# Performance work log

Hardware: AMD Instinct MI355X
Metric: run time of the kernel (lower is better)

## Reference

```python
import jax, jax.numpy as jnp
import numpy as np

# --- constants matching init_kwargs / input_specs ---
B, T, N, C = 16, 60, 196, 512
SEGS, TOP_K, TOP_M = 10, 6, 12
HEADS = 4
HD = C // HEADS  # 128
CLIP = T // SEGS  # 6
FRAMES = CLIP * TOP_K  # 36
LN_EPS = 1e-5


def setup_inputs() -> dict:
    key = jax.random.key(0)
    ks = jax.random.split(key, 16)
    s = 0.02
    return {
        "audio_feat": jax.random.normal(ks[0], (B, T, C), jnp.float32),
        "patch_feat": jax.random.normal(ks[1], (B, T, N, C), jnp.float32),
        "qst_feat": jax.random.normal(ks[2], (B, C), jnp.float32),
        "top_k_index_sort": jnp.sort(jax.random.randint(ks[3], (B, 1, TOP_K), 0, SEGS), axis=-1),
        # MultiheadAttention params (torch layout: in_proj [3C, C])
        "in_proj_w": jax.random.normal(ks[4], (3 * C, C), jnp.float32) * s,
        "in_proj_b": jnp.zeros((3 * C,), jnp.float32),
        "out_w": jax.random.normal(ks[5], (C, C), jnp.float32) * s,
        "out_b": jnp.zeros((C,), jnp.float32),
        # FFN
        "lin1_w": jax.random.normal(ks[6], (C, C), jnp.float32) * s,
        "lin1_b": jnp.zeros((C,), jnp.float32),
        "lin2_w": jax.random.normal(ks[7], (C, C), jnp.float32) * s,
        "lin2_b": jnp.zeros((C,), jnp.float32),
        # LayerNorm
        "ln_g": jnp.ones((C,), jnp.float32),
        "ln_b": jnp.zeros((C,), jnp.float32),
    }


def _layernorm(x, g, b):
    mu = jnp.mean(x, axis=-1, keepdims=True)
    var = jnp.mean(jnp.square(x - mu), axis=-1, keepdims=True)
    return (x - mu) * jax.lax.rsqrt(var + LN_EPS) * g + b


def _forward(audio_feat, patch_feat, qst_feat, top_k_index_sort,
             in_proj_w, in_proj_b, out_w, out_b,
             lin1_w, lin1_b, lin2_w, lin2_b, ln_g, ln_b):
    # --- TopKSegs: gather top-k temporal segments (clip_len frames each) ---
    seg_idx = top_k_index_sort[:, 0, :]  # [B, K]
    frame_ids = (seg_idx[:, :, None] * CLIP + jnp.arange(CLIP)[None, None, :]).reshape(B, FRAMES)
    audio_top_k = jnp.take_along_axis(audio_feat, frame_ids[:, :, None], axis=1)            # [B, F, C]
    patch_top_k = jnp.take_along_axis(patch_feat, frame_ids[:, :, None, None], axis=1)      # [B, F, N, C]

    # --- QstQueryPatchAttn: batched cross-attention (q_len=1 per frame) ---
    Wq, Wk, Wv = in_proj_w[:C], in_proj_w[C:2 * C], in_proj_w[2 * C:]
    bq, bk, bv = in_proj_b[:C], in_proj_b[C:2 * C], in_proj_b[2 * C:]
    q = (qst_feat @ Wq.T + bq).reshape(B, HEADS, HD)                    # [B, h, d]
    k = (patch_top_k @ Wk.T + bk).reshape(B, FRAMES, N, HEADS, HD)      # [B, F, N, h, d]
    v = (patch_top_k @ Wv.T + bv).reshape(B, FRAMES, N, HEADS, HD)
    scale = 1.0 / jnp.sqrt(jnp.asarray(HD, jnp.float32))
    scores = jnp.einsum('bhd,bfnhd->bfhn', q, k) * scale                # [B, F, h, N]
    w = jax.nn.softmax(scores, axis=-1)
    ctx = jnp.einsum('bfhn,bfnhd->bfhd', w, v).reshape(B, FRAMES, C)
    attn_feat = ctx @ out_w.T + out_b                                   # [B, F, C]
    patch_weights = jnp.mean(w, axis=2)                                 # [B, F, N] (avg heads)

    src = jax.nn.relu(attn_feat @ lin1_w.T + lin1_b) @ lin2_w.T + lin2_b
    visual_spatial_feat = _layernorm(attn_feat + src, ln_g, ln_b)       # computed but unused downstream

    # --- SelectTopM (faithful to original loop semantics):
    # top-m indices are sorted ascending and iterated with full-slab overwrite,
    sort_index = jnp.argsort(patch_weights, axis=-1)
    top_m_index = sort_index[:, :, -TOP_M:]
    top_m_index_sort = jnp.sort(top_m_index, axis=-1)
    pid = top_m_index_sort[0, 0, -1]  # last iterated patch id
    sel = jnp.take(patch_top_k, pid, axis=2)                            # [B, F, C]
    visual_patch_top_m = jnp.broadcast_to(sel[:, :, None, :], (B, FRAMES, TOP_M, C))
    visual_patch_feat = visual_patch_top_m.reshape(B, FRAMES * TOP_M, C)
    return audio_top_k, visual_patch_top_m, visual_patch_feat


def reference(audio_feat, patch_feat, qst_feat, top_k_index_sort,
              in_proj_w, in_proj_b, out_w, out_b,
              lin1_w, lin1_b, lin2_w, lin2_b, ln_g, ln_b):
    return _forward(audio_feat, patch_feat, qst_feat, top_k_index_sort,
                    in_proj_w, in_proj_b, out_w, out_b,
                    lin1_w, lin1_b, lin2_w, lin2_b, ln_g, ln_b)
```

## Files before the change

kernel.cpp:

```cpp
#include <hip/hip_runtime.h>
#include <math.h>

#define B_     16
#define T_     60
#define N_     196
#define C_     512
#define SEGS_  10
#define TOPK_  6
#define TOPM_  12
#define HEADS_ 4
#define HD_    128
#define CLIP_  6
#define FRAMES_ 36

#define WS_Q    0
#define WS_SCP  512
#define WS_PID  2080

#define SCALE_ 0.08838834764831845f

__global__ void qproj_kernel(const float* __restrict__ qst,
                             const float* __restrict__ ipw,
                             const float* __restrict__ ipb,
                             float* __restrict__ ws) {
    __shared__ float x[C_];
    int tid = threadIdx.x;
    x[tid]       = qst[tid];
    x[tid + 256] = qst[tid + 256];
    __syncthreads();

    int wave = tid >> 6, lane = tid & 63;
    int half = lane >> 5, l = lane & 31;
    int row = blockIdx.x * 8 + wave * 2 + half;

    const float4* w4 = (const float4*)(ipw + (size_t)row * C_);
    const float4* x4 = (const float4*)x;
    float acc = 0.f;
    #pragma unroll
    for (int j = 0; j < 4; ++j) {
        float4 wv = w4[l + 32 * j];
        float4 xv = x4[l + 32 * j];
        acc += wv.x * xv.x + wv.y * xv.y + wv.z * xv.z + wv.w * xv.w;
    }
    for (int off = 16; off; off >>= 1) acc += __shfl_xor(acc, off);
    if (l == 0) ws[WS_Q + row] = acc + ipb[row];
}

__global__ void score_kernel(const float* __restrict__ patch,
                             const int* __restrict__ tk,
                             const float* __restrict__ ipw,
                             float* __restrict__ ws) {
    __shared__ float qh[HD_];
    __shared__ float us[256];
    int tid = threadIdx.x;
    int h = blockIdx.x >> 1, half = blockIdx.x & 1;
    int c = half * 256 + tid;

    if (tid < HD_) qh[tid] = ws[WS_Q + h * HD_ + tid];
    __syncthreads();

    const float* wk = ipw + (size_t)(C_ + h * HD_) * C_ + c;
    float u = 0.f;
    #pragma unroll 16
    for (int d = 0; d < HD_; ++d) u += qh[d] * wk[(size_t)d * C_];
    us[tid] = u;
    __syncthreads();

    int fid0 = tk[0] * CLIP_;
    const float* pb = patch + (size_t)fid0 * N_ * C_ + half * 256;
    int wave = tid >> 6, lane = tid & 63;
    const float4* u4 = (const float4*)us;
    float4 uv = u4[lane];
    for (int n = wave; n < N_; n += 4) {
        const float4* x4 = (const float4*)(pb + (size_t)n * C_);
        float4 xv = x4[lane];
        float p = uv.x * xv.x + uv.y * xv.y + uv.z * xv.z + uv.w * xv.w;
        for (int off = 32; off; off >>= 1) p += __shfl_down(p, off);
        if (lane == 0)
            ws[WS_SCP + (size_t)blockIdx.x * N_ + n] = p * SCALE_;
    }
}

__global__ void pid_kernel(float* __restrict__ ws) {
    __shared__ float wgt[HEADS_][N_];
    __shared__ float pw[N_];
    int tid = threadIdx.x;
    int h = tid >> 6, j = tid & 63;

    float sc[4]; float ex[4];
    int m = 0;
    float mx = -1e30f;
    for (int n = j; n < N_; n += 64) {
        sc[m] = ws[WS_SCP + (size_t)(2 * h) * N_ + n]
              + ws[WS_SCP + (size_t)(2 * h + 1) * N_ + n];
        mx = fmaxf(mx, sc[m]);
        ++m;
    }
    for (int off = 1; off < 64; off <<= 1) mx = fmaxf(mx, __shfl_xor(mx, off));
    float sum = 0.f;
    for (int s = 0; s < m; ++s) { ex[s] = expf(sc[s] - mx); sum += ex[s]; }
    for (int off = 1; off < 64; off <<= 1) sum += __shfl_xor(sum, off);
    float inv = 1.f / sum;
    m = 0;
    for (int n = j; n < N_; n += 64) { wgt[h][n] = ex[m] * inv; ++m; }
    __syncthreads();

    for (int n = tid; n < N_; n += 256)
        pw[n] = 0.25f * (wgt[0][n] + wgt[1][n] + wgt[2][n] + wgt[3][n]);
    __syncthreads();

    if (tid < 64) {
        float v[4];
        for (int s = 0; s < 4; ++s) {
            int n = j + 64 * s;
            v[s] = (n < N_) ? pw[n] : -1e30f;
        }
        int pid = -1;
        for (int r = 0; r < TOPM_; ++r) {
            float bv = -1e30f; int bi = -1;
            for (int s = 0; s < 4; ++s) {
                int n = j + 64 * s;
                if (v[s] > bv || (v[s] == bv && n > bi)) { bv = v[s]; bi = n; }
            }
            for (int off = 1; off < 64; off <<= 1) {
                float ov = __shfl_xor(bv, off);
                int   oi = __shfl_xor(bi, off);
                if (ov > bv || (ov == bv && oi > bi)) { bv = ov; bi = oi; }
            }
            if ((bi & 63) == j) v[bi >> 6] = -1e30f;
            if (bi > pid) pid = bi;
        }
        if (j == 0) ((int*)ws)[WS_PID] = pid;
    }
}

__global__ void out_kernel(const float* __restrict__ audio,
                           const float* __restrict__ patch,
                           const int* __restrict__ tk,
                           const float* __restrict__ ws,
                           float* __restrict__ out) {
    int bf = blockIdx.x;
    int b = bf / FRAMES_, f = bf % FRAMES_;
    int k = f / CLIP_, c = f % CLIP_;
    int fid = tk[b * TOPK_ + k] * CLIP_ + c;
    int t = threadIdx.x;
    int pid = ((const int*)ws)[WS_PID];

    const float4* a4 = (const float4*)(audio + ((size_t)b * T_ + fid) * C_);
    const float4* p4 = (const float4*)(patch + (((size_t)b * T_ + fid) * N_ + pid) * C_);
    float4 av = a4[t];
    float4 sv = p4[t];

    float4* o0 = (float4*)out;
    float4* o1 = (float4*)(out + (size_t)B_ * FRAMES_ * C_);
    float4* o2 = (float4*)(out + (size_t)B_ * FRAMES_ * C_ + (size_t)B_ * FRAMES_ * TOPM_ * C_);

    o0[(size_t)bf * (C_ / 4) + t] = av;
    size_t rb = (size_t)bf * TOPM_ * (C_ / 4);
    #pragma unroll
    for (int mm = 0; mm < TOPM_; ++mm) {
        o1[rb + mm * (C_ / 4) + t] = sv;
        o2[rb + mm * (C_ / 4) + t] = sv;
    }
}

extern "C" void kernel_launch(void* const* d_in, const int* in_sizes, int n_in,
                              void* d_out, int out_size, void* d_ws, size_t ws_size,
                              hipStream_t stream) {
    const float* audio = (const float*)d_in[0];
    const float* patch = (const float*)d_in[1];
    const float* qst   = (const float*)d_in[2];
    const int*   tk    = (const int*)d_in[3];
    const float* ipw   = (const float*)d_in[4];
    const float* ipb   = (const float*)d_in[5];
    float* out = (float*)d_out;
    float* ws  = (float*)d_ws;

    qproj_kernel<<<64, 256, 0, stream>>>(qst, ipw, ipb, ws);
    score_kernel<<<8, 256, 0, stream>>>(patch, tk, ipw, ws);
    pid_kernel<<<1, 256, 0, stream>>>(ws);
    out_kernel<<<B_ * FRAMES_, 128, 0, stream>>>(audio, patch, tk, ws, out);
}
```

Before: 497.1 us.

## Fuse pid selection into output kernel and split score work across more blocks

The single-block pid kernel is removed: every output block now redundantly recomputes the softmax, head averaging and top-M selection from the score partials, which drops one launch and its serialization. The score kernel is split into 16 blocks, each covering a quarter of the channels with the head dimension split in two, so more CUs share the key-projection and patch dot-product work. The output kernel runs 256 threads per block, each half writing six of the twelve replicated rows. The cost is redundant pid computation in all 576 blocks before any output is written.

```diff
diff --git a/kernel.cpp b/kernel.cpp
--- a/kernel.cpp
+++ b/kernel.cpp
@@ -15,7 +15,7 @@
 
 #define WS_Q    0
 #define WS_SCP  512
-#define WS_PID  2080
+#define WS_PID  3648
 
 #define SCALE_ 0.08838834764831845f
 
@@ -51,39 +51,49 @@
                              const float* __restrict__ ipw,
                              float* __restrict__ ws) {
     __shared__ float qh[HD_];
-    __shared__ float us[256];
+    __shared__ float upart[2][128];
+    __shared__ float us[128];
     int tid = threadIdx.x;
-    int h = blockIdx.x >> 1, half = blockIdx.x & 1;
-    int c = half * 256 + tid;
+    int h = blockIdx.x >> 2, qt = blockIdx.x & 3;
 
     if (tid < HD_) qh[tid] = ws[WS_Q + h * HD_ + tid];
     __syncthreads();
 
-    const float* wk = ipw + (size_t)(C_ + h * HD_) * C_ + c;
+    int c = tid & 127;
+    int dh = tid >> 7;
+    const float* wk = ipw + (size_t)(C_ + h * HD_ + dh * 64) * C_ + qt * 128 + c;
     float u = 0.f;
     #pragma unroll 16
-    for (int d = 0; d < HD_; ++d) u += qh[d] * wk[(size_t)d * C_];
-    us[tid] = u;
+    for (int d = 0; d < 64; ++d) u += qh[dh * 64 + d] * wk[(size_t)d * C_];
+    upart[dh][c] = u;
+    __syncthreads();
+    if (tid < 128) us[tid] = upart[0][tid] + upart[1][tid];
     __syncthreads();
 
     int fid0 = tk[0] * CLIP_;
-    const float* pb = patch + (size_t)fid0 * N_ * C_ + half * 256;
+    const float* pb = patch + (size_t)fid0 * N_ * C_ + qt * 128;
     int wave = tid >> 6, lane = tid & 63;
+    int g = lane >> 5, l = lane & 31;
     const float4* u4 = (const float4*)us;
-    float4 uv = u4[lane];
-    for (int n = wave; n < N_; n += 4) {
+    float4 uv = u4[l];
+    for (int n = wave * 2 + g; n < N_; n += 8) {
         const float4* x4 = (const float4*)(pb + (size_t)n * C_);
-        float4 xv = x4[lane];
+        float4 xv = x4[l];
         float p = uv.x * xv.x + uv.y * xv.y + uv.z * xv.z + uv.w * xv.w;
-        for (int off = 32; off; off >>= 1) p += __shfl_down(p, off);
-        if (lane == 0)
+        for (int off = 16; off; off >>= 1) p += __shfl_xor(p, off);
+        if (l == 0)
             ws[WS_SCP + (size_t)blockIdx.x * N_ + n] = p * SCALE_;
     }
 }
 
-__global__ void pid_kernel(float* __restrict__ ws) {
+__global__ void out_kernel(const float* __restrict__ audio,
+                           const float* __restrict__ patch,
+                           const int* __restrict__ tk,
+                           const float* __restrict__ ws,
+                           float* __restrict__ out) {
     __shared__ float wgt[HEADS_][N_];
     __shared__ float pw[N_];
+    __shared__ int pid_s;
     int tid = threadIdx.x;
     int h = tid >> 6, j = tid & 63;
 
@@ -91,9 +101,12 @@
     int m = 0;
     float mx = -1e30f;
     for (int n = j; n < N_; n += 64) {
-        sc[m] = ws[WS_SCP + (size_t)(2 * h) * N_ + n]
-              + ws[WS_SCP + (size_t)(2 * h + 1) * N_ + n];
-        mx = fmaxf(mx, sc[m]);
+        float s = ws[WS_SCP + (size_t)(h * 4 + 0) * N_ + n]
+                + ws[WS_SCP + (size_t)(h * 4 + 1) * N_ + n]
+                + ws[WS_SCP + (size_t)(h * 4 + 2) * N_ + n]
+                + ws[WS_SCP + (size_t)(h * 4 + 3) * N_ + n];
+        sc[m] = s;
+        mx = fmaxf(mx, s);
         ++m;
     }
     for (int off = 1; off < 64; off <<= 1) mx = fmaxf(mx, __shfl_xor(mx, off));
@@ -130,37 +143,35 @@
             if ((bi & 63) == j) v[bi >> 6] = -1e30f;
             if (bi > pid) pid = bi;
         }
-        if (j == 0) ((int*)ws)[WS_PID] = pid;
+        if (tid == 0) pid_s = pid;
     }
-}
+    __syncthreads();
+    int pid = pid_s;
 
-__global__ void out_kernel(const float* __restrict__ audio,
-                           const float* __restrict__ patch,
-                           const int* __restrict__ tk,
-                           const float* __restrict__ ws,
-                           float* __restrict__ out) {
     int bf = blockIdx.x;
     int b = bf / FRAMES_, f = bf % FRAMES_;
     int k = f / CLIP_, c = f % CLIP_;
     int fid = tk[b * TOPK_ + k] * CLIP_ + c;
-    int t = threadIdx.x;
-    int pid = ((const int*)ws)[WS_PID];
+    int t = tid & 127;
+    int half = tid >> 7;
 
-    const float4* a4 = (const float4*)(audio + ((size_t)b * T_ + fid) * C_);
     const float4* p4 = (const float4*)(patch + (((size_t)b * T_ + fid) * N_ + pid) * C_);
-    float4 av = a4[t];
     float4 sv = p4[t];
 
     float4* o0 = (float4*)out;
     float4* o1 = (float4*)(out + (size_t)B_ * FRAMES_ * C_);
     float4* o2 = (float4*)(out + (size_t)B_ * FRAMES_ * C_ + (size_t)B_ * FRAMES_ * TOPM_ * C_);
 
-    o0[(size_t)bf * (C_ / 4) + t] = av;
+    if (half == 0) {
+        const float4* a4 = (const float4*)(audio + ((size_t)b * T_ + fid) * C_);
+        o0[(size_t)bf * (C_ / 4) + t] = a4[t];
+    }
     size_t rb = (size_t)bf * TOPM_ * (C_ / 4);
     #pragma unroll
-    for (int mm = 0; mm < TOPM_; ++mm) {
-        o1[rb + mm * (C_ / 4) + t] = sv;
-        o2[rb + mm * (C_ / 4) + t] = sv;
+    for (int mm = 0; mm < 6; ++mm) {
+        int m2 = half * 6 + mm;
+        o1[rb + m2 * (C_ / 4) + t] = sv;
+        o2[rb + m2 * (C_ / 4) + t] = sv;
     }
 }
 
@@ -177,7 +188,6 @@
     float* ws  = (float*)d_ws;
 
     qproj_kernel<<<64, 256, 0, stream>>>(qst, ipw, ipb, ws);
-    score_kernel<<<8, 256, 0, stream>>>(patch, tk, ipw, ws);
-    pid_kernel<<<1, 256, 0, stream>>>(ws);
-    out_kernel<<<B_ * FRAMES_, 128, 0, stream>>>(audio, patch, tk, ws, out);
+    score_kernel<<<16, 256, 0, stream>>>(patch, tk, ipw, ws);
+    out_kernel<<<B_ * FRAMES_, 256, 0, stream>>>(audio, patch, tk, ws, out);
 }
```

Result: faster. 474.8 us (-4.5%).
